# Optimization experiments

Hardware: AMD Instinct MI355X
Metric: run time of the kernel (lower is better)

## Reference

```python
import jax, jax.numpy as jnp
import numpy as np

B, L, C, V = 16, 600, 256, 256
OUT_SEQ = 6000
KSZ = 5
DILATIONS = (1, 2, 4)
N_BLOCKS = 10
COND = 256  # speaker(128) + noise(128)
TEMP = 10.0
EPS = 1e-5


def _ccbn(x, cond, gw, gb, bw, bb):
    # x: (B, C, L); conditional batch-norm: per-channel stats over (batch, length),
    # gamma/beta predicted from condition vector.
    mu = jnp.mean(x, axis=(0, 2), keepdims=True)
    var = jnp.var(x, axis=(0, 2), keepdims=True)
    xn = (x - mu) * jax.lax.rsqrt(var + EPS)
    gamma = 1.0 + cond @ gw + gb  # (B, C)
    beta = cond @ bw + bb         # (B, C)
    return xn * gamma[:, :, None] + beta[:, :, None]


def _conv1d(x, w, b, dil=1):
    # x: (B, C_in, L); w: (C_out, C_in, K)
    y = jax.lax.conv_general_dilated(
        x, w, window_strides=(1,), padding='SAME', rhs_dilation=(dil,),
        dimension_numbers=('NCH', 'OIH', 'NCH'))
    return y + b[None, :, None]


def setup_inputs() -> dict:
    key = jax.random.key(0)
    ks = jax.random.split(key, 20)
    s = 0.02
    inp = {
        'inputs': jax.random.randint(ks[0], (B, L), 0, V),
        'speaker_embeddings': jax.random.normal(ks[1], (B, 128), jnp.float32),
        'noise': jax.random.normal(ks[2], (B, 128), jnp.float32),
        'emb': jax.random.normal(ks[3], (V, C), jnp.float32) * s,
        # 10 blocks x 3 dilated convs
        'conv_w': jax.random.normal(ks[4], (N_BLOCKS, 3, C, C, KSZ), jnp.float32) * s,
        'conv_b': jnp.zeros((N_BLOCKS, 3, C), jnp.float32),
        # CCBN projections per conv (gamma/beta from condition)
        'g_w': jax.random.normal(ks[5], (N_BLOCKS, 3, COND, C), jnp.float32) * s,
        'g_b': jnp.zeros((N_BLOCKS, 3, C), jnp.float32),
        'b_w': jax.random.normal(ks[6], (N_BLOCKS, 3, COND, C), jnp.float32) * s,
        'b_b': jnp.zeros((N_BLOCKS, 3, C), jnp.float32),
        # TokenLength head: 2 CCBNs + conv1 (256->256,k1) + conv2 (256->1,k1)
        'tl_g_w': jax.random.normal(ks[7], (2, COND, C), jnp.float32) * s,
        'tl_g_b': jnp.zeros((2, C), jnp.float32),
        'tl_b_w': jax.random.normal(ks[8], (2, COND, C), jnp.float32) * s,
        'tl_b_b': jnp.zeros((2, C), jnp.float32),
        'tl_conv1_w': jax.random.normal(ks[9], (C, C, 1), jnp.float32) * s,
        'tl_conv1_b': jnp.zeros((C,), jnp.float32),
        'tl_conv2_w': jax.random.normal(ks[10], (1, C, 1), jnp.float32) * s,
        'tl_conv2_b': jnp.zeros((1,), jnp.float32),
    }
    return inp


def reference(inputs, speaker_embeddings, noise, emb, conv_w, conv_b,
              g_w, g_b, b_w, b_b, tl_g_w, tl_g_b, tl_b_w, tl_b_b,
              tl_conv1_w, tl_conv1_b, tl_conv2_w, tl_conv2_b):
    cond = jnp.concatenate([speaker_embeddings, noise], axis=-1)  # (B, COND)
    x = emb[inputs]                    # (B, L, C)
    x = jnp.transpose(x, (0, 2, 1))    # (B, C, L)

    # 10 unaligned blocks: residual stacks of CCBN -> ReLU -> dilated conv
    for blk in range(N_BLOCKS):
        y = x
        for j, d in enumerate(DILATIONS):
            y = jax.nn.relu(_ccbn(y, cond, g_w[blk, j], g_b[blk, j], b_w[blk, j], b_b[blk, j]))
            y = _conv1d(y, conv_w[blk, j], conv_b[blk, j], dil=d)
        x = x + y
    unaligned = x  # (B, C, L)

    # TokenLength head
    t = jax.nn.relu(_ccbn(unaligned, cond, tl_g_w[0], tl_g_b[0], tl_b_w[0], tl_b_b[0]))
    t = _conv1d(t, tl_conv1_w, tl_conv1_b)
    t = jax.nn.relu(_ccbn(t, cond, tl_g_w[1], tl_g_b[1], tl_b_w[1], tl_b_b[1]))
    t = _conv1d(t, tl_conv2_w, tl_conv2_b)  # (B, 1, L)
    token_lengths = jax.nn.relu(t[:, 0, :])  # (B, L)

    token_ends = jnp.cumsum(token_lengths, axis=-1)        # (B, L)
    token_centers = token_ends - token_lengths / 2.0        # (B, L)
    aligned_lengths = token_ends

    out_pos = jnp.arange(OUT_SEQ, dtype=jnp.float32)         # (OUT,)
    diff = token_centers[:, None, :] - out_pos[None, :, None]  # (B, OUT, L)
    logits = -(diff * diff) / TEMP
    weights = jax.nn.softmax(logits, axis=-1)                # (B, OUT, L)

    feats = jnp.transpose(unaligned, (0, 2, 1))              # (B, L, C)
    aligned_features = jnp.einsum('bol,blc->boc', weights, feats)  # (B, OUT, C)
    return aligned_features, aligned_lengths
```

## Files before the change

### kernel.cpp

```cpp
#include <hip/hip_runtime.h>
#include <math.h>
#include <stdint.h>

#define EPSv 1e-5f

typedef short short8 __attribute__((ext_vector_type(8)));
typedef float floatx4 __attribute__((ext_vector_type(4)));

__device__ __forceinline__ unsigned short f2bf(float x) {
  unsigned u = __float_as_uint(x);
  unsigned r = (u + 0x7fffu + ((u >> 16) & 1u)) >> 16;
  return (unsigned short)r;
}

__device__ __forceinline__ void gld_lds16(const void* g, void* l) {
  __builtin_amdgcn_global_load_lds(
      (const __attribute__((address_space(1))) unsigned*)(uintptr_t)g,
      (__attribute__((address_space(3))) unsigned*)(uintptr_t)l,
      16, 0, 0);
}

__global__ void k_gamma_beta(const float* __restrict__ spk, const float* __restrict__ noise,
                             const float* __restrict__ g_w, const float* __restrict__ g_b,
                             const float* __restrict__ b_w, const float* __restrict__ b_b,
                             const float* __restrict__ tl_g_w, const float* __restrict__ tl_g_b,
                             const float* __restrict__ tl_b_w, const float* __restrict__ tl_b_b,
                             float* __restrict__ gammas, float* __restrict__ betas) {
  __shared__ float condl[16*256];
  int t = threadIdx.x;
  for (int idx = t; idx < 4096; idx += 256) {
    int b = idx >> 8, k = idx & 255;
    condl[idx] = (k < 128) ? spk[b*128 + k] : noise[b*128 + k - 128];
  }
  __syncthreads();
  int i = blockIdx.x;
  const float *gw, *bw, *gbias, *bbias;
  if (i < 30) { gw = g_w + (size_t)i*65536; bw = b_w + (size_t)i*65536; gbias = g_b + i*256; bbias = b_b + i*256; }
  else { int j = i - 30; gw = tl_g_w + (size_t)j*65536; bw = tl_b_w + (size_t)j*65536; gbias = tl_g_b + j*256; bbias = tl_b_b + j*256; }
  int co = (t & 63) + blockIdx.y * 64;
  int slot = t >> 6;
  float g[4] = {0.f,0.f,0.f,0.f}, bt[4] = {0.f,0.f,0.f,0.f};
  for (int k = 0; k < 256; ++k) {
    float gwv = gw[k*256 + co];
    float bwv = bw[k*256 + co];
    #pragma unroll
    for (int bb = 0; bb < 4; ++bb) {
      float cv = condl[(slot*4 + bb)*256 + k];
      g[bb]  = fmaf(cv, gwv, g[bb]);
      bt[bb] = fmaf(cv, bwv, bt[bb]);
    }
  }
  #pragma unroll
  for (int bb = 0; bb < 4; ++bb) {
    int b = slot*4 + bb;
    gammas[i*4096 + b*256 + co] = 1.0f + g[bb] + gbias[co];
    betas [i*4096 + b*256 + co] = bt[bb] + bbias[co];
  }
}

template<int TAPS>
__device__ __forceinline__ void wprep_body(const float* __restrict__ src,
                                           unsigned short* __restrict__ dst,
                                           int cotile, int chunk, int t) {
  int cow = t >> 2, ci8 = (t & 3) * 8;
  const float* s0 = src + ((size_t)(cotile*64 + cow)*256 + chunk*32 + ci8)*TAPS;
  float v[8*TAPS];
  #pragma unroll
  for (int i = 0; i < 8*TAPS; ++i) v[i] = s0[i];
  unsigned short* dblk = dst + (size_t)cotile*(8*TAPS*4096) + (size_t)chunk*(TAPS*4096);
  #pragma unroll
  for (int tap = 0; tap < TAPS; ++tap) {
    unsigned hi2[4], lo2[4];
    #pragma unroll
    for (int jj = 0; jj < 4; ++jj) {
      float a = v[(jj*2+0)*TAPS + tap], b = v[(jj*2+1)*TAPS + tap];
      unsigned short ha = f2bf(a), hb = f2bf(b);
      unsigned short la = f2bf(a - __uint_as_float((unsigned)ha << 16));
      unsigned short lb = f2bf(b - __uint_as_float((unsigned)hb << 16));
      hi2[jj] = (unsigned)ha | ((unsigned)hb << 16);
      lo2[jj] = (unsigned)la | ((unsigned)lb << 16);
    }
    uint4 H; H.x = hi2[0]; H.y = hi2[1]; H.z = hi2[2]; H.w = hi2[3];
    uint4 L; L.x = lo2[0]; L.y = lo2[1]; L.z = lo2[2]; L.w = lo2[3];
    *(uint4*)(dblk + (size_t)(tap*2)*2048 + cow*32 + ci8) = H;
    *(uint4*)(dblk + (size_t)(tap*2+1)*2048 + cow*32 + ci8) = L;
  }
}

__global__ __launch_bounds__(256) void k_wprep(const float* __restrict__ conv_w,
                                               const float* __restrict__ tl_c1_w,
                                               unsigned short* __restrict__ wp) {
  int cc = blockIdx.x;
  int cotile = blockIdx.y >> 3, chunk = blockIdx.y & 7;
  if (cc == 30) wprep_body<1>(tl_c1_w, wp + (size_t)30*655360, cotile, chunk, threadIdx.x);
  else          wprep_body<5>(conv_w + (size_t)cc*327680, wp + (size_t)cc*655360, cotile, chunk, threadIdx.x);
}

__global__ void k_embed2(const int* __restrict__ inp, const float* __restrict__ emb,
                         float* __restrict__ x, float* __restrict__ statp) {
  int bx = blockIdx.x;
  int c = threadIdx.x;
  int r0 = bx * 60;
  float s = 0.f, s2 = 0.f;
  for (int r = 0; r < 60; ++r) {
    int row = inp[r0 + r];
    float v = emb[(size_t)row*256 + c];
    x[(size_t)(r0 + r)*256 + c] = v;
    s += v; s2 = fmaf(v, v, s2);
  }
  statp[(size_t)bx*512 + c] = s;
  statp[(size_t)bx*512 + 256 + c] = s2;
}

__global__ __launch_bounds__(256) void k_norm(const float* __restrict__ z,
                      const float* __restrict__ statp,
                      const float* __restrict__ gam, const float* __restrict__ bet,
                      unsigned short* __restrict__ zn) {
  __shared__ float s_sc[32];
  __shared__ float s_sh[32];
  __shared__ float red[2][32][8];
  int b = blockIdx.x, chunk = blockIdx.y, rg = blockIdx.z;
  int t = threadIdx.x;
  {
    int ch = t >> 3, g = t & 7;
    int c = chunk*32 + ch;
    float s = 0.f, s2 = 0.f;
    for (int p = g; p < 160; p += 8) {
      s  += statp[(size_t)p*512 + c];
      s2 += statp[(size_t)p*512 + 256 + c];
    }
    red[0][ch][g] = s; red[1][ch][g] = s2;
  }
  __syncthreads();
  if (t < 32) {
    float s = 0.f, s2 = 0.f;
    #pragma unroll
    for (int g = 0; g < 8; ++g) { s += red[0][t][g]; s2 += red[1][t][g]; }
    int c = chunk*32 + t;
    float mu = s * (1.0f/9600.0f);
    float var = s2 * (1.0f/9600.0f) - mu*mu;
    float rs = rsqrtf(var + EPSv);
    float scale = rs * gam[b*256 + c];
    s_sc[t] = scale;
    s_sh[t] = fmaf(-mu, scale, bet[b*256 + c]);
  }
  __syncthreads();
  int srow = t >> 3, fq = t & 7;
  float4 sc4 = *(const float4*)&s_sc[fq*4];
  float4 sh4 = *(const float4*)&s_sh[fq*4];
  unsigned short* zh = zn + ((size_t)b*8 + chunk)*54400 + fq*4;
  unsigned short* zl = zh + 27200;
  const float* zb = z + (size_t)b*600*256 + chunk*32 + fq*4;
  #pragma unroll
  for (int i = 0; i < 4; ++i) {
    int r = rg*128 + i*32 + srow;
    if (r < 680) {
      int l = r - 8;
      uint2 vh; vh.x = 0u; vh.y = 0u;
      uint2 vl; vl.x = 0u; vl.y = 0u;
      if (l >= 0 && l < 600) {
        float4 zv = *(const float4*)&zb[(size_t)l*256];
        float v0 = fmaxf(fmaf(zv.x, sc4.x, sh4.x), 0.f);
        float v1 = fmaxf(fmaf(zv.y, sc4.y, sh4.y), 0.f);
        float v2 = fmaxf(fmaf(zv.z, sc4.z, sh4.z), 0.f);
        float v3 = fmaxf(fmaf(zv.w, sc4.w, sh4.w), 0.f);
        unsigned short h0 = f2bf(v0), h1 = f2bf(v1), h2 = f2bf(v2), h3 = f2bf(v3);
        unsigned short e0 = f2bf(v0 - __uint_as_float((unsigned)h0 << 16));
        unsigned short e1 = f2bf(v1 - __uint_as_float((unsigned)h1 << 16));
        unsigned short e2 = f2bf(v2 - __uint_as_float((unsigned)h2 << 16));
        unsigned short e3 = f2bf(v3 - __uint_as_float((unsigned)h3 << 16));
        vh.x = (unsigned)h0 | ((unsigned)h1 << 16);
        vh.y = (unsigned)h2 | ((unsigned)h3 << 16);
        vl.x = (unsigned)e0 | ((unsigned)e1 << 16);
        vl.y = (unsigned)e2 | ((unsigned)e3 << 16);
      }
      *(uint2*)&zh[(size_t)r*40] = vh;
      *(uint2*)&zl[(size_t)r*40] = vl;
    }
  }
}

template<int TAPS>
__global__ __launch_bounds__(256) void k_convm(const unsigned short* __restrict__ zn,
                        float* __restrict__ out, float* __restrict__ statp,
                        const unsigned short* __restrict__ wpc,
                        const float* __restrict__ bias, int dil, int mode) {
  __shared__ __align__(16) unsigned short Zhi[2][3584];
  __shared__ __align__(16) unsigned short Zlo[2][3584];
  __shared__ float lsum[32];
  __shared__ float lsq[32];
  int t = threadIdx.x;
  int bx = blockIdx.x;
  int b  = bx / 10;
  int l0 = (bx % 10) * 64;
  int co0 = blockIdx.y * 32;
  int cobase = (blockIdx.y & 1) * 32;
  int PAD = ((TAPS - 1)/2) * dil;
  int w = t >> 6, lane = t & 63;
  int lsub = (w & 1) * 32, cosub = (w >> 1) * 16;
  int quad = lane >> 4, nlan = lane & 15;
  if (t < 32) { lsum[t] = 0.f; lsq[t] = 0.f; }

  floatx4 acc[2];
  acc[0] = (floatx4){0.f,0.f,0.f,0.f};
  acc[1] = (floatx4){0.f,0.f,0.f,0.f};

  const unsigned short* zbase = zn + (size_t)b*435200 + (size_t)(l0 - PAD + 8)*40 + (size_t)lane*8;
  int ar0 = (lsub + nlan) * 40 + quad * 8;
  int ar1 = ar0 + 640;

  #define STAGE(ch, bf) do {                                            \
    const unsigned short* srcp = zbase + (size_t)(ch)*54400;            \
    for (int i = w; i < 14; i += 4) {                                   \
      int p = (i >= 7) ? 1 : 0;                                         \
      int k = i - p*7;                                                  \
      gld_lds16(srcp + p*27200 + k*512, (p ? Zlo[bf] : Zhi[bf]) + k*512); \
    }                                                                   \
  } while (0)

  STAGE(0, 0);
  __syncthreads();

  for (int chunk = 0; chunk < 8; ++chunk) {
    int cb = chunk & 1;
    if (chunk < 7) STAGE(chunk + 1, cb ^ 1);
    const unsigned short* pch = wpc + (size_t)((blockIdx.y >> 1)*8 + chunk) * (TAPS*4096);
    short8 bh[TAPS], bl[TAPS];
    int cw = (cobase + cosub + nlan)*32 + quad*8;
    #pragma unroll
    for (int tap = 0; tap < TAPS; ++tap) {
      bh[tap] = *(const short8*)(pch + (size_t)(tap*2)*2048 + cw);
      bl[tap] = *(const short8*)(pch + (size_t)(tap*2+1)*2048 + cw);
    }
    #pragma unroll
    for (int tap = 0; tap < TAPS; ++tap) {
      int sh = tap * dil * 40;
      short8 ah0 = *(const short8*)&Zhi[cb][ar0 + sh];
      short8 ah1 = *(const short8*)&Zhi[cb][ar1 + sh];
      short8 al0 = *(const short8*)&Zlo[cb][ar0 + sh];
      short8 al1 = *(const short8*)&Zlo[cb][ar1 + sh];
      acc[0] = __builtin_amdgcn_mfma_f32_16x16x32_bf16(ah0, bh[tap], acc[0], 0, 0, 0);
      acc[0] = __builtin_amdgcn_mfma_f32_16x16x32_bf16(ah0, bl[tap], acc[0], 0, 0, 0);
      acc[0] = __builtin_amdgcn_mfma_f32_16x16x32_bf16(al0, bh[tap], acc[0], 0, 0, 0);
      acc[1] = __builtin_amdgcn_mfma_f32_16x16x32_bf16(ah1, bh[tap], acc[1], 0, 0, 0);
      acc[1] = __builtin_amdgcn_mfma_f32_16x16x32_bf16(ah1, bl[tap], acc[1], 0, 0, 0);
      acc[1] = __builtin_amdgcn_mfma_f32_16x16x32_bf16(al1, bh[tap], acc[1], 0, 0, 0);
    }
    __syncthreads();
  }
  #undef STAGE

  float bsv = bias[co0 + cosub + nlan];
  float ssum = 0.f, ssq = 0.f;
  #pragma unroll
  for (int mt = 0; mt < 2; ++mt) {
    #pragma unroll
    for (int r = 0; r < 4; ++r) {
      int l = l0 + lsub + mt*16 + quad*4 + r;
      if (l < 600) {
        float v = acc[mt][r] + bsv;
        float* dst = &out[((size_t)(b*600 + l))*256 + co0 + cosub + nlan];
        if (mode) v += *dst;
        *dst = v;
        ssum += v;
        ssq = fmaf(v, v, ssq);
      }
    }
  }
  ssum += __shfl_xor(ssum, 16, 64);
  ssum += __shfl_xor(ssum, 32, 64);
  ssq  += __shfl_xor(ssq, 16, 64);
  ssq  += __shfl_xor(ssq, 32, 64);
  if (quad == 0) {
    atomicAdd(&lsum[cosub + nlan], ssum);
    atomicAdd(&lsq [cosub + nlan], ssq);
  }
  __syncthreads();
  if (t < 32) {
    statp[(size_t)bx*512 + co0 + t] = lsum[t];
    statp[(size_t)bx*512 + 256 + co0 + t] = lsq[t];
  }
}

__global__ void k_statred(const float* __restrict__ sp, float* __restrict__ dst) {
  int idx = blockIdx.x*256 + threadIdx.x;
  float s = 0.f;
  for (int p = 0; p < 160; ++p) s += sp[(size_t)p*512 + idx];
  dst[idx] = s;
}

__global__ void k_tl2(const float* __restrict__ z, const float* __restrict__ stat,
                      const float* __restrict__ gam, const float* __restrict__ bet,
                      const float* __restrict__ w2, const float* __restrict__ b2,
                      float* __restrict__ tl) {
  int t = threadIdx.x;
  int row = blockIdx.x * 4 + (t >> 6);
  int lane = t & 63;
  int b = row / 600;
  float4 s1 = *(const float4*)&stat[lane*4];
  float4 s2 = *(const float4*)&stat[256 + lane*4];
  float4 gm = *(const float4*)&gam[b*256 + lane*4];
  float4 bt = *(const float4*)&bet[b*256 + lane*4];
  float sc[4], sh[4];
  {
    float sv[4] = {s1.x, s1.y, s1.z, s1.w};
    float qv[4] = {s2.x, s2.y, s2.z, s2.w};
    float gv[4] = {gm.x, gm.y, gm.z, gm.w};
    float bv[4] = {bt.x, bt.y, bt.z, bt.w};
    #pragma unroll
    for (int i = 0; i < 4; ++i) {
      float mu = sv[i] * (1.0f/9600.0f);
      float var = qv[i] * (1.0f/9600.0f) - mu*mu;
      float rs = rsqrtf(var + EPSv);
      sc[i] = rs * gv[i];
      sh[i] = fmaf(-mu, sc[i], bv[i]);
    }
  }
  float4 zr = *(const float4*)&z[(size_t)row*256 + lane*4];
  float4 wr = *(const float4*)&w2[lane*4];
  float z0 = fmaxf(fmaf(zr.x, sc[0], sh[0]), 0.f);
  float z1 = fmaxf(fmaf(zr.y, sc[1], sh[1]), 0.f);
  float z2 = fmaxf(fmaf(zr.z, sc[2], sh[2]), 0.f);
  float z3 = fmaxf(fmaf(zr.w, sc[3], sh[3]), 0.f);
  float s = z0*wr.x + z1*wr.y + z2*wr.z + z3*wr.w;
  for (int m = 32; m >= 1; m >>= 1) s += __shfl_xor(s, m, 64);
  if (lane == 0) tl[row] = fmaxf(s + b2[0], 0.f);
}

__global__ void k_cumsum(const float* __restrict__ tl, float* __restrict__ centers,
                         float* __restrict__ out_len) {
  int b = blockIdx.x; int lane = threadIdx.x;
  float carry = 0.f;
  for (int ch = 0; ch < 10; ++ch) {
    int l = ch*64 + lane;
    float v = (l < 600) ? tl[b*600 + l] : 0.f;
    float s = v;
    #pragma unroll
    for (int off = 1; off < 64; off <<= 1) {
      float n = __shfl_up(s, off, 64);
      if (lane >= off) s += n;
    }
    float ends = carry + s;
    if (l < 600) {
      centers[b*600 + l] = ends - 0.5f*v;
      out_len[b*600 + l] = ends;
    }
    carry = __shfl(ends, 63, 64);
  }
}

__global__ void k_tobf16(const float* __restrict__ x, unsigned short* __restrict__ fbT) {
  __shared__ unsigned short T[64*66];
  int b = blockIdx.x, lt = blockIdx.y, ct = blockIdx.z;
  int t = threadIdx.x;
  int i4 = t >> 6;
  int j = t & 63;
  #pragma unroll
  for (int r = 0; r < 16; ++r) {
    int li = i4*16 + r;
    int l = lt*64 + li;
    float v = (l < 600) ? x[((size_t)(b*600 + l))*256 + ct*64 + j] : 0.f;
    T[j*66 + li] = f2bf(v);
  }
  __syncthreads();
  int row = t >> 2, seg = (t & 3) * 16;
  unsigned vv[8];
  #pragma unroll
  for (int k = 0; k < 8; ++k)
    vv[k] = *(const unsigned*)&T[row*66 + seg + k*2];
  size_t dsth = ((size_t)(b*256 + ct*64 + row))*640 + lt*64 + seg;
  unsigned* du = (unsigned*)fbT;
  uint4 a; a.x = vv[0]; a.y = vv[1]; a.z = vv[2]; a.w = vv[3];
  uint4 c4; c4.x = vv[4]; c4.y = vv[5]; c4.z = vv[6]; c4.w = vv[7];
  *(uint4*)(du + dsth/2) = a;
  *(uint4*)(du + dsth/2 + 4) = c4;
}

__global__ __launch_bounds__(256, 4) void k_align2(const unsigned short* __restrict__ fbT,
                        const float* __restrict__ centers, float* __restrict__ outp) {
  __shared__ float cen[600];
  __shared__ float mrow[64];
  __shared__ float isum[64];
  __shared__ unsigned short Wt[2][64*72];
  int b = blockIdx.x;
  int o0 = blockIdx.y * 64;
  int t = threadIdx.x;
  int wv = t >> 6, lane = t & 63;
  for (int i = t; i < 600; i += 256) cen[i] = centers[b*600 + i];
  __syncthreads();
  for (int rr = 0; rr < 16; ++rr) {
    int oi = wv*16 + rr;
    float opos = (float)(o0 + oi);
    float mx = -3.0e38f;
    for (int l = lane; l < 600; l += 64) {
      float d = cen[l] - opos;
      mx = fmaxf(mx, -d*d*0.1f);
    }
    #pragma unroll
    for (int mm = 32; mm >= 1; mm >>= 1) mx = fmaxf(mx, __shfl_xor(mx, mm, 64));
    if (lane == 0) mrow[oi] = mx;
  }
  __syncthreads();
  floatx4 acc[4][4];
  #pragma unroll
  for (int i = 0; i < 4; ++i)
    #pragma unroll
    for (int j = 0; j < 4; ++j)
      acc[i][j] = (floatx4){0.f, 0.f, 0.f, 0.f};
  int quad = lane >> 4;
  int nlan = lane & 15;
  int oi_w = t >> 2;
  int sbase = t & 3;
  float mo = mrow[oi_w];
  float opos_w = (float)(o0 + oi_w);
  float psum = 0.f;
  const unsigned short* srcb = fbT + ((size_t)b*256)*640;
  const unsigned short* fbl = srcb + (size_t)(wv*64 + nlan)*640 + quad*8;

  #define STAGE_WT(CH, BF) do {                                              \
    int lcs = (CH) * 64;                                                     \
    _Pragma("unroll")                                                        \
    for (int sidx = 0; sidx < 2; ++sidx) {                                   \
      int seg = sbase + sidx*4;                                              \
      unsigned pk[4];                                                        \
      _Pragma("unroll")                                                      \
      for (int jj = 0; jj < 8; jj += 2) {                                    \
        int li = lcs + seg*8 + jj;                                           \
        float e0 = 0.f, e1 = 0.f;                                            \
        if (li < 600)     { float d = cen[li] - opos_w;     e0 = __expf(-d*d*0.1f - mo); } \
        if (li + 1 < 600) { float d = cen[li + 1] - opos_w; e1 = __expf(-d*d*0.1f - mo); } \
        psum += e0 + e1;                                                     \
        pk[jj>>1] = (unsigned)f2bf(e0) | ((unsigned)f2bf(e1) << 16);         \
      }                                                                      \
      uint4 v; v.x = pk[0]; v.y = pk[1]; v.z = pk[2]; v.w = pk[3];           \
      *(uint4*)&Wt[BF][oi_w*72 + seg*8] = v;                                 \
    }                                                                        \
  } while (0)

  STAGE_WT(0, 0);
  __syncthreads();

  for (int ch = 0; ch < 10; ++ch) {
    int rb = ch & 1;
    int lc0 = ch * 64;
    short8 bfr[2][4];
    #pragma unroll
    for (int ks = 0; ks < 2; ++ks)
      #pragma unroll
      for (int nt = 0; nt < 4; ++nt)
        bfr[ks][nt] = *(const short8*)(fbl + (size_t)nt*16*640 + lc0 + ks*32);
    if (ch < 9) STAGE_WT(ch + 1, rb ^ 1);
    #pragma unroll
    for (int ks = 0; ks < 2; ++ks) {
      int ko = ks*32 + quad*8;
      short8 af[4];
      #pragma unroll
      for (int mt = 0; mt < 4; ++mt)
        af[mt] = *(const short8*)&Wt[rb][(mt*16 + nlan)*72 + ko];
      #pragma unroll
      for (int mt = 0; mt < 4; ++mt)
        #pragma unroll
        for (int nt = 0; nt < 4; ++nt)
          acc[mt][nt] = __builtin_amdgcn_mfma_f32_16x16x32_bf16(af[mt], bfr[ks][nt], acc[mt][nt], 0, 0, 0);
    }
    __syncthreads();
  }
  #undef STAGE_WT

  psum += __shfl_xor(psum, 1, 64);
  psum += __shfl_xor(psum, 2, 64);
  if ((t & 3) == 0) isum[oi_w] = 1.0f / psum;
  __syncthreads();
  #pragma unroll
  for (int mt = 0; mt < 4; ++mt) {
    #pragma unroll
    for (int r = 0; r < 4; ++r) {
      int oi = mt*16 + quad*4 + r;
      int o = o0 + oi;
      if (o < 6000) {
        float sc = isum[oi];
        #pragma unroll
        for (int nt = 0; nt < 4; ++nt) {
          int c = wv*64 + nt*16 + nlan;
          outp[((size_t)b*6000 + o)*256 + c] = acc[mt][nt][r] * sc;
        }
      }
    }
  }
}

extern "C" void kernel_launch(void* const* d_in, const int* in_sizes, int n_in,
                              void* d_out, int out_size, void* d_ws, size_t ws_size,
                              hipStream_t stream) {
  const int*   inputs = (const int*)  d_in[0];
  const float* spk    = (const float*)d_in[1];
  const float* noise  = (const float*)d_in[2];
  const float* emb    = (const float*)d_in[3];
  const float* conv_w = (const float*)d_in[4];
  const float* conv_b = (const float*)d_in[5];
  const float* g_w    = (const float*)d_in[6];
  const float* g_b    = (const float*)d_in[7];
  const float* b_w    = (const float*)d_in[8];
  const float* b_b    = (const float*)d_in[9];
  const float* tl_g_w = (const float*)d_in[10];
  const float* tl_g_b = (const float*)d_in[11];
  const float* tl_b_w = (const float*)d_in[12];
  const float* tl_b_b = (const float*)d_in[13];
  const float* tl_c1_w = (const float*)d_in[14];
  const float* tl_c1_b = (const float*)d_in[15];
  const float* tl_c2_w = (const float*)d_in[16];
  const float* tl_c2_b = (const float*)d_in[17];
  float* out = (float*)d_out;

  float* ws = (float*)d_ws;
  float* x       = ws;
  float* A       = x + 2457600;
  float* Bf      = A + 2457600;
  float* gammas  = Bf + 2457600;
  float* betas   = gammas + 131072;
  float* statp   = betas + 131072;
  float* stat31  = statp + 81920;
  float* tl      = stat31 + 512;
  float* cen     = tl + 9600;
  unsigned short* wp = (unsigned short*)(cen + 9600);
  unsigned short* Zn = wp + (size_t)31*655360;
  unsigned short* fbT = (unsigned short*)Bf;

  k_wprep<<<dim3(31, 32), dim3(256), 0, stream>>>(conv_w, tl_c1_w, wp);
  k_gamma_beta<<<dim3(32, 4), dim3(256), 0, stream>>>(spk, noise, g_w, g_b, b_w, b_b,
      tl_g_w, tl_g_b, tl_b_w, tl_b_b, gammas, betas);
  k_embed2<<<dim3(160), dim3(256), 0, stream>>>(inputs, emb, x, statp);

  const int dils[3] = {1, 2, 4};
  for (int blk = 0; blk < 10; ++blk) {
    const float* srcs[3] = {x, A, Bf};
    float*       dsts[3] = {A, Bf, x};
    for (int j = 0; j < 3; ++j) {
      int idx = blk*3 + j;
      int mode = (j == 2) ? 1 : 0;
      k_norm<<<dim3(16, 8, 6), dim3(256), 0, stream>>>(srcs[j],
          statp, gammas + idx*4096, betas + idx*4096, Zn);
      k_convm<5><<<dim3(160, 8), dim3(256), 0, stream>>>(Zn, dsts[j],
          statp, wp + (size_t)idx*655360, conv_b + idx*256, dils[j], mode);
    }
  }
  k_norm<<<dim3(16, 8, 6), dim3(256), 0, stream>>>(x,
      statp, gammas + 30*4096, betas + 30*4096, Zn);
  k_convm<1><<<dim3(160, 8), dim3(256), 0, stream>>>(Zn, A,
      statp, wp + (size_t)30*655360, tl_c1_b, 1, 0);
  k_statred<<<dim3(2), dim3(256), 0, stream>>>(statp, stat31);
  k_tl2<<<dim3(2400), dim3(256), 0, stream>>>(A, stat31,
      gammas + 31*4096, betas + 31*4096, tl_c2_w, tl_c2_b, tl);
  k_cumsum<<<dim3(16), dim3(64), 0, stream>>>(tl, cen, out + 24576000);
  k_tobf16<<<dim3(16, 10, 4), dim3(256), 0, stream>>>(x, fbT);
  k_align2<<<dim3(16, 94), dim3(256), 0, stream>>>(fbT, cen, out);
}
```

Before: 1.760 ms.

## Double conv L-tile to 128 rows per block and pad alignment LDS stride

Measured after the change: 1.616 ms. -8.2%, faster.

```diff
diff --git a/kernel.cpp b/kernel.cpp
--- a/kernel.cpp
+++ b/kernel.cpp
@@ -100,9 +100,9 @@
                          float* __restrict__ x, float* __restrict__ statp) {
   int bx = blockIdx.x;
   int c = threadIdx.x;
-  int r0 = bx * 60;
+  int r0 = bx * 120;
   float s = 0.f, s2 = 0.f;
-  for (int r = 0; r < 60; ++r) {
+  for (int r = 0; r < 120; ++r) {
     int row = inp[r0 + r];
     float v = emb[(size_t)row*256 + c];
     x[(size_t)(r0 + r)*256 + c] = v;
@@ -119,13 +119,13 @@
   __shared__ float s_sc[32];
   __shared__ float s_sh[32];
   __shared__ float red[2][32][8];
-  int b = blockIdx.x, chunk = blockIdx.y, rg = blockIdx.z;
+  int b = blockIdx.x, chunk = blockIdx.y, sub = blockIdx.z;
   int t = threadIdx.x;
   {
     int ch = t >> 3, g = t & 7;
     int c = chunk*32 + ch;
     float s = 0.f, s2 = 0.f;
-    for (int p = g; p < 160; p += 8) {
+    for (int p = g; p < 80; p += 8) {
       s  += statp[(size_t)p*512 + c];
       s2 += statp[(size_t)p*512 + 256 + c];
     }
@@ -151,10 +151,12 @@
   unsigned short* zh = zn + ((size_t)b*8 + chunk)*54400 + fq*4;
   unsigned short* zl = zh + 27200;
   const float* zb = z + (size_t)b*600*256 + chunk*32 + fq*4;
-  #pragma unroll
-  for (int i = 0; i < 4; ++i) {
-    int r = rg*128 + i*32 + srow;
-    if (r < 680) {
+  int r0 = sub*68;
+  #pragma unroll
+  for (int i = 0; i < 3; ++i) {
+    int rr = i*32 + srow;
+    if (rr < 68) {
+      int r = r0 + rr;
       int l = r - 8;
       uint2 vh; vh.x = 0u; vh.y = 0u;
       uint2 vl; vl.x = 0u; vl.y = 0u;
@@ -181,50 +183,52 @@
 }
 
 template<int TAPS>
-__global__ __launch_bounds__(256) void k_convm(const unsigned short* __restrict__ zn,
+__global__ __launch_bounds__(256, 3) void k_convm(const unsigned short* __restrict__ zn,
                         float* __restrict__ out, float* __restrict__ statp,
                         const unsigned short* __restrict__ wpc,
                         const float* __restrict__ bias, int dil, int mode) {
-  __shared__ __align__(16) unsigned short Zhi[2][3584];
-  __shared__ __align__(16) unsigned short Zlo[2][3584];
+  __shared__ __align__(16) unsigned short Zhi[2][6144];
+  __shared__ __align__(16) unsigned short Zlo[2][6144];
   __shared__ float lsum[32];
   __shared__ float lsq[32];
   int t = threadIdx.x;
   int bx = blockIdx.x;
-  int b  = bx / 10;
-  int l0 = (bx % 10) * 64;
-  int co0 = blockIdx.y * 32;
-  int cobase = (blockIdx.y & 1) * 32;
+  int b  = bx / 5;
+  int l0 = (bx % 5) * 128;
+  int y = blockIdx.y;
+  int co0 = y * 32;
+  int cobase = (y & 1) * 32;
   int PAD = ((TAPS - 1)/2) * dil;
   int w = t >> 6, lane = t & 63;
-  int lsub = (w & 1) * 32, cosub = (w >> 1) * 16;
+  int lsub = (w & 1) * 64, cosub = (w >> 1) * 16;
   int quad = lane >> 4, nlan = lane & 15;
   if (t < 32) { lsum[t] = 0.f; lsq[t] = 0.f; }
 
-  floatx4 acc[2];
-  acc[0] = (floatx4){0.f,0.f,0.f,0.f};
-  acc[1] = (floatx4){0.f,0.f,0.f,0.f};
+  floatx4 acc[4];
+  #pragma unroll
+  for (int mt = 0; mt < 4; ++mt) acc[mt] = (floatx4){0.f,0.f,0.f,0.f};
 
   const unsigned short* zbase = zn + (size_t)b*435200 + (size_t)(l0 - PAD + 8)*40 + (size_t)lane*8;
-  int ar0 = (lsub + nlan) * 40 + quad * 8;
-  int ar1 = ar0 + 640;
-
-  #define STAGE(ch, bf) do {                                            \
-    const unsigned short* srcp = zbase + (size_t)(ch)*54400;            \
-    for (int i = w; i < 14; i += 4) {                                   \
-      int p = (i >= 7) ? 1 : 0;                                         \
-      int k = i - p*7;                                                  \
+  int ar[4];
+  #pragma unroll
+  for (int mt = 0; mt < 4; ++mt) ar[mt] = (lsub + mt*16 + nlan) * 40 + quad * 8;
+
+  #define STAGEZ(ch, bf) do {                                             \
+    const unsigned short* srcp = zbase + (size_t)(ch)*54400;              \
+    for (int i = w; i < 24; i += 4) {                                     \
+      int p = (i >= 12) ? 1 : 0;                                          \
+      int k = i - p*12;                                                   \
       gld_lds16(srcp + p*27200 + k*512, (p ? Zlo[bf] : Zhi[bf]) + k*512); \
-    }                                                                   \
+    }                                                                     \
   } while (0)
 
-  STAGE(0, 0);
+  STAGEZ(0, 0);
   __syncthreads();
 
   for (int chunk = 0; chunk < 8; ++chunk) {
     int cb = chunk & 1;
-    if (chunk < 7) STAGE(chunk + 1, cb ^ 1);
-    const unsigned short* pch = wpc + (size_t)((blockIdx.y >> 1)*8 + chunk) * (TAPS*4096);
+    if (chunk < 7) STAGEZ(chunk + 1, cb ^ 1);
+    const unsigned short* pch = wpc + (size_t)((y >> 1)*8 + chunk) * (TAPS*4096);
     short8 bh[TAPS], bl[TAPS];
     int cw = (cobase + cosub + nlan)*32 + quad*8;
     #pragma unroll
@@ -235,25 +239,23 @@
     #pragma unroll
     for (int tap = 0; tap < TAPS; ++tap) {
       int sh = tap * dil * 40;
-      short8 ah0 = *(const short8*)&Zhi[cb][ar0 + sh];
-      short8 ah1 = *(const short8*)&Zhi[cb][ar1 + sh];
-      short8 al0 = *(const short8*)&Zlo[cb][ar0 + sh];
-      short8 al1 = *(const short8*)&Zlo[cb][ar1 + sh];
-      acc[0] = __builtin_amdgcn_mfma_f32_16x16x32_bf16(ah0, bh[tap], acc[0], 0, 0, 0);
-      acc[0] = __builtin_amdgcn_mfma_f32_16x16x32_bf16(ah0, bl[tap], acc[0], 0, 0, 0);
-      acc[0] = __builtin_amdgcn_mfma_f32_16x16x32_bf16(al0, bh[tap], acc[0], 0, 0, 0);
-      acc[1] = __builtin_amdgcn_mfma_f32_16x16x32_bf16(ah1, bh[tap], acc[1], 0, 0, 0);
-      acc[1] = __builtin_amdgcn_mfma_f32_16x16x32_bf16(ah1, bl[tap], acc[1], 0, 0, 0);
-      acc[1] = __builtin_amdgcn_mfma_f32_16x16x32_bf16(al1, bh[tap], acc[1], 0, 0, 0);
+      #pragma unroll
+      for (int mt = 0; mt < 4; ++mt) {
+        short8 ah = *(const short8*)&Zhi[cb][ar[mt] + sh];
+        short8 al = *(const short8*)&Zlo[cb][ar[mt] + sh];
+        acc[mt] = __builtin_amdgcn_mfma_f32_16x16x32_bf16(ah, bh[tap], acc[mt], 0, 0, 0);
+        acc[mt] = __builtin_amdgcn_mfma_f32_16x16x32_bf16(ah, bl[tap], acc[mt], 0, 0, 0);
+        acc[mt] = __builtin_amdgcn_mfma_f32_16x16x32_bf16(al, bh[tap], acc[mt], 0, 0, 0);
+      }
     }
     __syncthreads();
   }
-  #undef STAGE
+  #undef STAGEZ
 
   float bsv = bias[co0 + cosub + nlan];
   float ssum = 0.f, ssq = 0.f;
   #pragma unroll
-  for (int mt = 0; mt < 2; ++mt) {
+  for (int mt = 0; mt < 4; ++mt) {
     #pragma unroll
     for (int r = 0; r < 4; ++r) {
       int l = l0 + lsub + mt*16 + quad*4 + r;
@@ -285,7 +287,7 @@
 __global__ void k_statred(const float* __restrict__ sp, float* __restrict__ dst) {
   int idx = blockIdx.x*256 + threadIdx.x;
   float s = 0.f;
-  for (int p = 0; p < 160; ++p) s += sp[(size_t)p*512 + idx];
+  for (int p = 0; p < 80; ++p) s += sp[(size_t)p*512 + idx];
   dst[idx] = s;
 }
 
@@ -381,7 +383,7 @@
   __shared__ float cen[600];
   __shared__ float mrow[64];
   __shared__ float isum[64];
-  __shared__ unsigned short Wt[2][64*72];
+  __shared__ unsigned short Wt[2][64*80];
   int b = blockIdx.x;
   int o0 = blockIdx.y * 64;
   int t = threadIdx.x;
@@ -433,7 +435,7 @@
         pk[jj>>1] = (unsigned)f2bf(e0) | ((unsigned)f2bf(e1) << 16);         \
       }                                                                      \
       uint4 v; v.x = pk[0]; v.y = pk[1]; v.z = pk[2]; v.w = pk[3];           \
-      *(uint4*)&Wt[BF][oi_w*72 + seg*8] = v;                                 \
+      *(uint4*)&Wt[BF][oi_w*80 + seg*8] = v;                                 \
     }                                                                        \
   } while (0)
 
@@ -456,7 +458,7 @@
       short8 af[4];
       #pragma unroll
       for (int mt = 0; mt < 4; ++mt)
-        af[mt] = *(const short8*)&Wt[rb][(mt*16 + nlan)*72 + ko];
+        af[mt] = *(const short8*)&Wt[rb][(mt*16 + nlan)*80 + ko];
       #pragma unroll
       for (int mt = 0; mt < 4; ++mt)
         #pragma unroll
@@ -529,7 +531,7 @@
   k_wprep<<<dim3(31, 32), dim3(256), 0, stream>>>(conv_w, tl_c1_w, wp);
   k_gamma_beta<<<dim3(32, 4), dim3(256), 0, stream>>>(spk, noise, g_w, g_b, b_w, b_b,
       tl_g_w, tl_g_b, tl_b_w, tl_b_b, gammas, betas);
-  k_embed2<<<dim3(160), dim3(256), 0, stream>>>(inputs, emb, x, statp);
+  k_embed2<<<dim3(80), dim3(256), 0, stream>>>(inputs, emb, x, statp);
 
   const int dils[3] = {1, 2, 4};
   for (int blk = 0; blk < 10; ++blk) {
@@ -538,15 +540,15 @@
     for (int j = 0; j < 3; ++j) {
       int idx = blk*3 + j;
       int mode = (j == 2) ? 1 : 0;
-      k_norm<<<dim3(16, 8, 6), dim3(256), 0, stream>>>(srcs[j],
+      k_norm<<<dim3(16, 8, 10), dim3(256), 0, stream>>>(srcs[j],
           statp, gammas + idx*4096, betas + idx*4096, Zn);
-      k_convm<5><<<dim3(160, 8), dim3(256), 0, stream>>>(Zn, dsts[j],
+      k_convm<5><<<dim3(80, 8), dim3(256), 0, stream>>>(Zn, dsts[j],
           statp, wp + (size_t)idx*655360, conv_b + idx*256, dils[j], mode);
     }
   }
-  k_norm<<<dim3(16, 8, 6), dim3(256), 0, stream>>>(x,
+  k_norm<<<dim3(16, 8, 10), dim3(256), 0, stream>>>(x,
       statp, gammas + 30*4096, betas + 30*4096, Zn);
-  k_convm<1><<<dim3(160, 8), dim3(256), 0, stream>>>(Zn, A,
+  k_convm<1><<<dim3(80, 8), dim3(256), 0, stream>>>(Zn, A,
       statp, wp + (size_t)30*655360, tl_c1_b, 1, 0);
   k_statred<<<dim3(2), dim3(256), 0, stream>>>(statp, stat31);
   k_tl2<<<dim3(2400), dim3(256), 0, stream>>>(A, stat31,
```
